# Kernel tuning notes

Hardware: AMD Instinct MI355X
Metric: run time of the kernel (lower is better)

The kernel has to match this reference:

```python
import jax, jax.numpy as jnp
import numpy as np

N_NODES = 100000


def gcn_conv(x, edge_index, W, b):
    """PyG GCNConv: out = D^-1/2 (A+I) D^-1/2 (X W) + b, edge weights = 1."""
    n = x.shape[0]
    h = x @ W  # [N, F_out]
    row, col = edge_index[0], edge_index[1]  # source -> target
    ones = jnp.ones(row.shape[0], dtype=x.dtype)
    # degree on A + I (self loop contributes 1)
    deg = jax.ops.segment_sum(ones, col, num_segments=n) + 1.0
    dinv = jax.lax.rsqrt(deg)  # deg >= 1 so no inf
    norm = dinv[row] * dinv[col]  # [E]
    agg = jax.ops.segment_sum(h[row] * norm[:, None], col, num_segments=n)
    agg = agg + h * (dinv * dinv)[:, None]  # self-loop term
    return agg + b


def setup_inputs() -> dict:
    key = jax.random.key(0)
    ks = jax.random.split(key, 8)
    E = 3200000
    F_in, H, C = 128, 16, 2
    x = jax.random.normal(ks[0], (N_NODES, F_in), dtype=jnp.float32)
    edge_index = jax.random.randint(ks[1], (2, E), 0, N_NODES, dtype=jnp.int64)
    W1 = jax.random.normal(ks[2], (F_in, H), dtype=jnp.float32) * (1.0 / np.sqrt(F_in))
    b1 = jnp.zeros((H,), jnp.float32)
    W2 = jax.random.normal(ks[3], (H, H), dtype=jnp.float32) * (1.0 / np.sqrt(H))
    b2 = jnp.zeros((H,), jnp.float32)
    fc1_W = jax.random.normal(ks[4], (2 * H, H), dtype=jnp.float32) * (1.0 / np.sqrt(2 * H))
    fc1_b = jnp.zeros((H,), jnp.float32)
    fc2_W = jax.random.normal(ks[5], (H, C), dtype=jnp.float32) * (1.0 / np.sqrt(H))
    fc2_b = jnp.zeros((C,), jnp.float32)
    return {"x": x, "edge_index": edge_index, "W1": W1, "b1": b1, "W2": W2,
            "b2": b2, "fc1_W": fc1_W, "fc1_b": fc1_b, "fc2_W": fc2_W, "fc2_b": fc2_b}


def reference(x, edge_index, W1, b1, W2, b2, fc1_W, fc1_b, fc2_W, fc2_b):
    h = jax.nn.relu(gcn_conv(x, edge_index, W1, b1))
    h = jax.nn.relu(gcn_conv(h, edge_index, W2, b2))
    row, col = edge_index[0], edge_index[1]
    ef = jnp.concatenate([h[row], h[col]], axis=1)  # [E, 32]
    ef = jax.nn.relu(ef @ fc1_W + fc1_b)
    logits = ef @ fc2_W + fc2_b  # [E, 2]
    return jax.nn.log_softmax(logits, axis=1)
```

## Files before the change

### kernel.cpp

```cpp
#include <hip/hip_runtime.h>
#include <hip/hip_fp16.h>
#include <cstdint>
#include <cstddef>

#define F_IN 128
#define HID 16
#define NBUK 1024
#define NPB  128
#define CHUNK 8192

__global__ void k_detect(const int* __restrict__ eidx, int* __restrict__ flag) {
    if (blockIdx.x == 0 && threadIdx.x == 0) {
        int all0 = 1;
        for (int i = 0; i < 64; ++i) {
            if (eidx[2 * i + 1] != 0) { all0 = 0; break; }
        }
        *flag = all0;
    }
}

__device__ __forceinline__ int ld_idx(const int* __restrict__ p, int e, int is64) {
    return is64 ? p[2 * e] : p[e];
}

__launch_bounds__(256)
__global__ void k_bhist(const int* __restrict__ eidx, int E,
                        const int* __restrict__ flag, int* __restrict__ ghist) {
    __shared__ int lh[NBUK];
    int t = threadIdx.x;
    for (int i = t; i < NBUK; i += 256) lh[i] = 0;
    __syncthreads();
    int base = blockIdx.x * CHUNK;
    int cnt = min(CHUNK, E - base);
    int is64 = *flag;
    const int* colp = eidx + ((size_t)E << is64);
    for (int i = t; i < cnt; i += 256)
        atomicAdd(&lh[ld_idx(colp, base + i, is64) >> 7], 1);
    __syncthreads();
    for (int i = t; i < NBUK; i += 256)
        if (lh[i]) atomicAdd(&ghist[i], lh[i]);
}

__global__ void k_bscan(const int* __restrict__ ghist, int E,
                        int* __restrict__ boff, int* __restrict__ gcur) {
    __shared__ int s[NBUK];
    int t = threadIdx.x;
    int v = ghist[t];
    s[t] = v;
    __syncthreads();
    for (int off = 1; off < NBUK; off <<= 1) {
        int a = (t >= off) ? s[t - off] : 0;
        __syncthreads();
        s[t] += a;
        __syncthreads();
    }
    int excl = s[t] - v;
    boff[t] = excl;
    gcur[t] = excl;
    if (t == NBUK - 1) boff[NBUK] = E;
}

__launch_bounds__(256)
__global__ void k_bscatter(const int* __restrict__ eidx, int E,
                           const int* __restrict__ flag,
                           int* __restrict__ gcur, uint32_t* __restrict__ pairs) {
    __shared__ int lh[NBUK];
    __shared__ int lcur[NBUK];
    int t = threadIdx.x;
    for (int i = t; i < NBUK; i += 256) lh[i] = 0;
    __syncthreads();
    int base = blockIdx.x * CHUNK;
    int cnt = min(CHUNK, E - base);
    int is64 = *flag;
    const int* rowp = eidx;
    const int* colp = eidx + ((size_t)E << is64);
    for (int i = t; i < cnt; i += 256)
        atomicAdd(&lh[ld_idx(colp, base + i, is64) >> 7], 1);
    __syncthreads();
    for (int i = t; i < NBUK; i += 256) {
        int c = lh[i];
        lcur[i] = c ? atomicAdd(&gcur[i], c) : 0;
    }
    __syncthreads();
    for (int i = t; i < cnt; i += 256) {
        int c = ld_idx(colp, base + i, is64);
        int r = ld_idx(rowp, base + i, is64);
        int buk = c >> 7;
        int pos = atomicAdd(&lcur[buk], 1);
        pairs[pos] = (uint32_t)r | ((uint32_t)(c & 127) << 20);
    }
}

__launch_bounds__(256)
__global__ void k_bsort(const uint32_t* __restrict__ pairs, const int* __restrict__ boff,
                        int* __restrict__ srcs, int* __restrict__ noff,
                        float* __restrict__ dinv, int n) {
    __shared__ int cnt[NPB];
    __shared__ int scn[NPB];
    int t = threadIdx.x;
    int b = blockIdx.x;
    if (t < NPB) cnt[t] = 0;
    __syncthreads();
    int beg = boff[b], end = boff[b + 1];
    for (int k = beg + t; k < end; k += 256)
        atomicAdd(&cnt[pairs[k] >> 20], 1);
    __syncthreads();
    if (t < NPB) scn[t] = cnt[t];
    __syncthreads();
    for (int off = 1; off < NPB; off <<= 1) {
        int v = 0;
        if (t < NPB && t >= off) v = scn[t - off];
        __syncthreads();
        if (t < NPB) scn[t] += v;
        __syncthreads();
    }
    if (t < NPB) {
        int node = b * NPB + t;
        int excl = scn[t] - cnt[t];
        if (node <= n) noff[node] = beg + excl;
        if (node < n)  dinv[node] = rsqrtf((float)cnt[t] + 1.0f);
        cnt[t] = beg + excl;
    }
    __syncthreads();
    for (int k = beg + t; k < end; k += 256) {
        uint32_t p = pairs[k];
        int pos = atomicAdd(&cnt[p >> 20], 1);
        srcs[pos] = (int)(p & 0xFFFFF);
    }
}

__launch_bounds__(256)
__global__ void k_gemm1(const float* __restrict__ x, const float* __restrict__ W1,
                        const float* __restrict__ dinv, __half* __restrict__ hs, int n) {
    __shared__ float Wt[16 * 132];
    for (int i = threadIdx.x; i < F_IN * HID; i += 256) {
        int k = i >> 4, j = i & 15;
        Wt[j * 132 + k] = W1[i];
    }
    __syncthreads();
    int row = blockIdx.x * 16 + (threadIdx.x >> 4);
    int j = threadIdx.x & 15;
    if (row >= n) return;
    const float4* xr = (const float4*)(x + (size_t)row * F_IN);
    float acc = 0.f;
#pragma unroll
    for (int kk = 0; kk < 32; ++kk) {
        float4 xv = xr[kk];
        float4 wv = *(const float4*)&Wt[j * 132 + 4 * kk];
        acc += xv.x * wv.x + xv.y * wv.y + xv.z * wv.z + xv.w * wv.w;
    }
    hs[(size_t)row * HID + j] = __float2half(acc * dinv[row]);
}

template <int EPI>
__launch_bounds__(256)
__global__ void k_layer(const int* __restrict__ srcs, const int* __restrict__ noff,
                        const __half* __restrict__ hs, const float* __restrict__ dinv,
                        const float* __restrict__ bias, const float* __restrict__ Wnext,
                        __half* __restrict__ out0, __half* __restrict__ out1) {
    __shared__ float Ws[512];
    __shared__ float bs[16];
    __shared__ float srow[16 * 17];
    int t = threadIdx.x;
    int nw = (EPI == 0) ? 256 : 512;
    for (int i = t; i < nw; i += 256) Ws[i] = Wnext[i];
    if (t < 16) bs[t] = bias[t];
    __syncthreads();

    int i = blockIdx.x * 16 + (t >> 4);
    int j = t & 15;
    int beg = noff[i], end = noff[i + 1];
    float acc = __half2float(hs[(size_t)i * HID + j]);

    int kb = beg;
    for (; kb + 16 <= end; kb += 16) {
        int idx = srcs[kb + j];
#pragma unroll
        for (int m = 0; m < 16; ++m) {
            int r = __shfl(idx, m, 16);
            acc += __half2float(hs[(size_t)r * HID + j]);
        }
    }
    if (kb < end) {
        int lim = end - kb;
        int idx = srcs[kb + ((j < lim) ? j : (lim - 1))];
        for (int m = 0; m < lim; ++m) {
            int r = __shfl(idx, m, 16);
            acc += __half2float(hs[(size_t)r * HID + j]);
        }
    }

    float di = dinv[i];
    float hrelu = fmaxf(acc * di + bs[j], 0.f);
    int ln = t >> 4;
    __syncthreads();
    srow[ln * 17 + j] = hrelu;
    __syncthreads();
    float a0 = 0.f, a1 = 0.f;
#pragma unroll
    for (int k = 0; k < 16; ++k) {
        float hv = srow[ln * 17 + k];
        a0 += hv * Ws[k * 16 + j];
        if (EPI == 1) a1 += hv * Ws[(16 + k) * 16 + j];
    }
    if (EPI == 0) {
        out0[(size_t)i * HID + j] = __float2half(a0 * di);
    } else {
        out0[(size_t)i * HID + j] = __float2half(a0);
        out1[(size_t)i * HID + j] = __float2half(a1);
    }
}

__launch_bounds__(256)
__global__ void k_edge(const int* __restrict__ eidx, int E, const int* __restrict__ flag,
                       const __half* __restrict__ u, const __half* __restrict__ v,
                       const float* __restrict__ fc1b, const float* __restrict__ fc2W,
                       const float* __restrict__ fc2b, float* __restrict__ out) {
    __shared__ float b1s[16], W2s[32], b2s[2];
    if (threadIdx.x < 16) b1s[threadIdx.x] = fc1b[threadIdx.x];
    if (threadIdx.x < 32) W2s[threadIdx.x] = fc2W[threadIdx.x];
    if (threadIdx.x < 2) b2s[threadIdx.x] = fc2b[threadIdx.x];
    __syncthreads();
    int e = blockIdx.x * blockDim.x + threadIdx.x;
    if (e >= E) return;
    int is64 = *flag;
    const int* rowp = eidx;
    const int* colp = eidx + ((size_t)E << is64);
    int r = ld_idx(rowp, e, is64);
    int c = ld_idx(colp, e, is64);
    const uint4* up = (const uint4*)(u + (size_t)r * HID);
    const uint4* vp = (const uint4*)(v + (size_t)c * HID);
    uint4 U0 = up[0], U1 = up[1], V0 = vp[0], V1 = vp[1];
    float l0 = b2s[0], l1 = b2s[1];
#define PROC(uw, vw, jb)                                                        \
    {                                                                           \
        float2 fu = __half22float2(*(__half2*)&(uw));                           \
        float2 fv = __half22float2(*(__half2*)&(vw));                           \
        float z = fmaxf(fu.x + fv.x + b1s[jb], 0.f);                            \
        l0 += z * W2s[2 * (jb)]; l1 += z * W2s[2 * (jb) + 1];                   \
        z = fmaxf(fu.y + fv.y + b1s[(jb) + 1], 0.f);                            \
        l0 += z * W2s[2 * (jb) + 2]; l1 += z * W2s[2 * (jb) + 3];               \
    }
    PROC(U0.x, V0.x, 0) PROC(U0.y, V0.y, 2) PROC(U0.z, V0.z, 4) PROC(U0.w, V0.w, 6)
    PROC(U1.x, V1.x, 8) PROC(U1.y, V1.y, 10) PROC(U1.z, V1.z, 12) PROC(U1.w, V1.w, 14)
#undef PROC
    float m = fmaxf(l0, l1);
    float e0 = __expf(l0 - m), e1 = __expf(l1 - m);
    float lse = m + __logf(e0 + e1);
    ((float2*)out)[e] = make_float2(l0 - lse, l1 - lse);
}

static inline size_t rnd4(size_t v) { return (v + 3) & ~(size_t)3; }

extern "C" void kernel_launch(void* const* d_in, const int* in_sizes, int n_in,
                              void* d_out, int out_size, void* d_ws, size_t ws_size,
                              hipStream_t stream) {
    const float* x    = (const float*)d_in[0];
    const int*   eidx = (const int*)d_in[1];
    const float* W1   = (const float*)d_in[2];
    const float* b1   = (const float*)d_in[3];
    const float* W2   = (const float*)d_in[4];
    const float* b2   = (const float*)d_in[5];
    const float* fc1W = (const float*)d_in[6];
    const float* fc1b = (const float*)d_in[7];
    const float* fc2W = (const float*)d_in[8];
    const float* fc2b = (const float*)d_in[9];

    const int n = in_sizes[0] / F_IN;
    const int E = in_sizes[1] / 2;
    const int NBLK_SORT = (E + CHUNK - 1) / CHUNK;
    const int NBLK_BUK  = (n + NPB - 1) / NPB;

    float* ws = (float*)d_ws;
    size_t a = 0;
    float*    dinv  = ws + a;              a += rnd4(n);
    uint32_t* pairs = (uint32_t*)(ws + a); a += rnd4(E);
    int*      srcs  = (int*)(ws + a);      a += rnd4(E);
    int*      noff  = (int*)(ws + a);      a += rnd4(n + 1);
    int*      boff  = (int*)(ws + a);      a += rnd4(NBUK + 1);
    int*      gcur  = (int*)(ws + a);      a += NBUK;
    int*      ghist = (int*)(ws + a);      a += NBUK;
    int*      flag  = (int*)(ws + a);      a += 4;
    __half*   hs1   = (__half*)(ws + a);   a += rnd4((size_t)n * HID / 2);
    __half*   hs2   = (__half*)(ws + a);   a += rnd4((size_t)n * HID / 2);
    __half*   ubuf  = (__half*)(ws + a);   a += rnd4((size_t)n * HID / 2);
    __half*   vbuf  = (__half*)(ws + a);   a += rnd4((size_t)n * HID / 2);
    float* out = (float*)d_out;

    k_detect<<<1, 64, 0, stream>>>(eidx, flag);

    hipMemsetAsync(ghist, 0, NBUK * sizeof(int), stream);
    k_bhist<<<NBLK_SORT, 256, 0, stream>>>(eidx, E, flag, ghist);
    k_bscan<<<1, NBUK, 0, stream>>>(ghist, E, boff, gcur);
    k_bscatter<<<NBLK_SORT, 256, 0, stream>>>(eidx, E, flag, gcur, pairs);
    k_bsort<<<NBLK_BUK, 256, 0, stream>>>(pairs, boff, srcs, noff, dinv, n);

    k_gemm1<<<(n + 15) / 16, 256, 0, stream>>>(x, W1, dinv, hs1, n);

    k_layer<0><<<n / 16, 256, 0, stream>>>(srcs, noff, hs1, dinv, b1, W2, hs2, nullptr);
    k_layer<1><<<n / 16, 256, 0, stream>>>(srcs, noff, hs2, dinv, b2, fc1W, ubuf, vbuf);
    k_edge<<<(E + 255) / 256, 256, 0, stream>>>(eidx, E, flag, ubuf, vbuf,
                                                fc1b, fc2W, fc2b, out);
}
```

Baseline: 271.5 us.

## Pack int32 edge list during scatter, use nontemporal accesses, coarsen sort buckets

During the bucket scatter pass, each edge's (row, col) is also written as a packed int32 pair into spare workspace. The edge MLP kernel then reads that packed array instead of the strided int64 edge_index, which cuts the bytes it pulls in. Most streaming loads and stores become nontemporal. Buckets are coarsened from 1024×128 nodes to 256×512 nodes, and the per-bucket sort now runs with 512 threads, so fewer global atomics are needed. A redundant barrier in the layer kernel is also dropped. The costs are an extra write of the edge list and fewer, larger blocks in the bucket sort, which may underfill the GPU.

```diff
diff --git a/kernel.cpp b/kernel.cpp
--- a/kernel.cpp
+++ b/kernel.cpp
@@ -5,9 +5,13 @@
 
 #define F_IN 128
 #define HID 16
-#define NBUK 1024
-#define NPB  128
+#define NBUK 256
+#define NPB  512
 #define CHUNK 8192
+
+typedef float f4v __attribute__((ext_vector_type(4)));
+typedef float f2v __attribute__((ext_vector_type(2)));
+typedef int   i2v __attribute__((ext_vector_type(2)));
 
 __global__ void k_detect(const int* __restrict__ eidx, int* __restrict__ flag) {
     if (blockIdx.x == 0 && threadIdx.x == 0) {
@@ -19,8 +23,9 @@
     }
 }
 
-__device__ __forceinline__ int ld_idx(const int* __restrict__ p, int e, int is64) {
-    return is64 ? p[2 * e] : p[e];
+__device__ __forceinline__ int ld_idx_nt(const int* __restrict__ p, int e, int is64) {
+    return is64 ? __builtin_nontemporal_load(&p[2 * e])
+                : __builtin_nontemporal_load(&p[e]);
 }
 
 __launch_bounds__(256)
@@ -28,17 +33,16 @@
                         const int* __restrict__ flag, int* __restrict__ ghist) {
     __shared__ int lh[NBUK];
     int t = threadIdx.x;
-    for (int i = t; i < NBUK; i += 256) lh[i] = 0;
+    if (t < NBUK) lh[t] = 0;
     __syncthreads();
     int base = blockIdx.x * CHUNK;
     int cnt = min(CHUNK, E - base);
     int is64 = *flag;
     const int* colp = eidx + ((size_t)E << is64);
     for (int i = t; i < cnt; i += 256)
-        atomicAdd(&lh[ld_idx(colp, base + i, is64) >> 7], 1);
-    __syncthreads();
-    for (int i = t; i < NBUK; i += 256)
-        if (lh[i]) atomicAdd(&ghist[i], lh[i]);
+        atomicAdd(&lh[ld_idx_nt(colp, base + i, is64) >> 9], 1);
+    __syncthreads();
+    if (t < NBUK && lh[t]) atomicAdd(&ghist[t], lh[t]);
 }
 
 __global__ void k_bscan(const int* __restrict__ ghist, int E,
@@ -63,11 +67,12 @@
 __launch_bounds__(256)
 __global__ void k_bscatter(const int* __restrict__ eidx, int E,
                            const int* __restrict__ flag,
-                           int* __restrict__ gcur, uint32_t* __restrict__ pairs) {
+                           int* __restrict__ gcur, uint32_t* __restrict__ pairs,
+                           i2v* __restrict__ epack) {
     __shared__ int lh[NBUK];
     __shared__ int lcur[NBUK];
     int t = threadIdx.x;
-    for (int i = t; i < NBUK; i += 256) lh[i] = 0;
+    if (t < NBUK) lh[t] = 0;
     __syncthreads();
     int base = blockIdx.x * CHUNK;
     int cnt = min(CHUNK, E - base);
@@ -75,23 +80,28 @@
     const int* rowp = eidx;
     const int* colp = eidx + ((size_t)E << is64);
     for (int i = t; i < cnt; i += 256)
-        atomicAdd(&lh[ld_idx(colp, base + i, is64) >> 7], 1);
-    __syncthreads();
-    for (int i = t; i < NBUK; i += 256) {
-        int c = lh[i];
-        lcur[i] = c ? atomicAdd(&gcur[i], c) : 0;
+        atomicAdd(&lh[ld_idx_nt(colp, base + i, is64) >> 9], 1);
+    __syncthreads();
+    if (t < NBUK) {
+        int c = lh[t];
+        lcur[t] = c ? atomicAdd(&gcur[t], c) : 0;
     }
     __syncthreads();
     for (int i = t; i < cnt; i += 256) {
-        int c = ld_idx(colp, base + i, is64);
-        int r = ld_idx(rowp, base + i, is64);
-        int buk = c >> 7;
+        int e = base + i;
+        int c = ld_idx_nt(colp, e, is64);
+        int r = ld_idx_nt(rowp, e, is64);
+        if (epack) {
+            i2v pk; pk.x = r; pk.y = c;
+            __builtin_nontemporal_store(pk, &epack[e]);
+        }
+        int buk = c >> 9;
         int pos = atomicAdd(&lcur[buk], 1);
-        pairs[pos] = (uint32_t)r | ((uint32_t)(c & 127) << 20);
-    }
-}
-
-__launch_bounds__(256)
+        pairs[pos] = (uint32_t)r | ((uint32_t)(c & (NPB - 1)) << 20);
+    }
+}
+
+__launch_bounds__(512)
 __global__ void k_bsort(const uint32_t* __restrict__ pairs, const int* __restrict__ boff,
                         int* __restrict__ srcs, int* __restrict__ noff,
                         float* __restrict__ dinv, int n) {
@@ -99,30 +109,27 @@
     __shared__ int scn[NPB];
     int t = threadIdx.x;
     int b = blockIdx.x;
-    if (t < NPB) cnt[t] = 0;
+    cnt[t] = 0;
     __syncthreads();
     int beg = boff[b], end = boff[b + 1];
-    for (int k = beg + t; k < end; k += 256)
+    for (int k = beg + t; k < end; k += 512)
         atomicAdd(&cnt[pairs[k] >> 20], 1);
     __syncthreads();
-    if (t < NPB) scn[t] = cnt[t];
+    scn[t] = cnt[t];
     __syncthreads();
     for (int off = 1; off < NPB; off <<= 1) {
-        int v = 0;
-        if (t < NPB && t >= off) v = scn[t - off];
+        int v = (t >= off) ? scn[t - off] : 0;
         __syncthreads();
-        if (t < NPB) scn[t] += v;
+        scn[t] += v;
         __syncthreads();
     }
-    if (t < NPB) {
-        int node = b * NPB + t;
-        int excl = scn[t] - cnt[t];
-        if (node <= n) noff[node] = beg + excl;
-        if (node < n)  dinv[node] = rsqrtf((float)cnt[t] + 1.0f);
-        cnt[t] = beg + excl;
-    }
-    __syncthreads();
-    for (int k = beg + t; k < end; k += 256) {
+    int node = b * NPB + t;
+    int excl = scn[t] - cnt[t];
+    if (node <= n) noff[node] = beg + excl;
+    if (node < n)  dinv[node] = rsqrtf((float)cnt[t] + 1.0f);
+    cnt[t] = beg + excl;
+    __syncthreads();
+    for (int k = beg + t; k < end; k += 512) {
         uint32_t p = pairs[k];
         int pos = atomicAdd(&cnt[p >> 20], 1);
         srcs[pos] = (int)(p & 0xFFFFF);
@@ -141,11 +148,11 @@
     int row = blockIdx.x * 16 + (threadIdx.x >> 4);
     int j = threadIdx.x & 15;
     if (row >= n) return;
-    const float4* xr = (const float4*)(x + (size_t)row * F_IN);
+    const f4v* xr = (const f4v*)(x + (size_t)row * F_IN);
     float acc = 0.f;
 #pragma unroll
     for (int kk = 0; kk < 32; ++kk) {
-        float4 xv = xr[kk];
+        f4v xv = __builtin_nontemporal_load(&xr[kk]);
         float4 wv = *(const float4*)&Wt[j * 132 + 4 * kk];
         acc += xv.x * wv.x + xv.y * wv.y + xv.z * wv.z + xv.w * wv.w;
     }
@@ -174,7 +181,7 @@
 
     int kb = beg;
     for (; kb + 16 <= end; kb += 16) {
-        int idx = srcs[kb + j];
+        int idx = __builtin_nontemporal_load(&srcs[kb + j]);
 #pragma unroll
         for (int m = 0; m < 16; ++m) {
             int r = __shfl(idx, m, 16);
@@ -193,7 +200,6 @@
     float di = dinv[i];
     float hrelu = fmaxf(acc * di + bs[j], 0.f);
     int ln = t >> 4;
-    __syncthreads();
     srow[ln * 17 + j] = hrelu;
     __syncthreads();
     float a0 = 0.f, a1 = 0.f;
@@ -211,8 +217,10 @@
     }
 }
 
-__launch_bounds__(256)
-__global__ void k_edge(const int* __restrict__ eidx, int E, const int* __restrict__ flag,
+template <int USE_EPACK>
+__launch_bounds__(256)
+__global__ void k_edge(const int* __restrict__ eidx, const i2v* __restrict__ epack,
+                       int E, const int* __restrict__ flag,
                        const __half* __restrict__ u, const __half* __restrict__ v,
                        const float* __restrict__ fc1b, const float* __restrict__ fc2W,
                        const float* __restrict__ fc2b, float* __restrict__ out) {
@@ -223,11 +231,17 @@
     __syncthreads();
     int e = blockIdx.x * blockDim.x + threadIdx.x;
     if (e >= E) return;
-    int is64 = *flag;
-    const int* rowp = eidx;
-    const int* colp = eidx + ((size_t)E << is64);
-    int r = ld_idx(rowp, e, is64);
-    int c = ld_idx(colp, e, is64);
+    int r, c;
+    if (USE_EPACK) {
+        i2v pk = __builtin_nontemporal_load(&epack[e]);
+        r = pk.x; c = pk.y;
+    } else {
+        int is64 = *flag;
+        const int* rowp = eidx;
+        const int* colp = eidx + ((size_t)E << is64);
+        r = ld_idx_nt(rowp, e, is64);
+        c = ld_idx_nt(colp, e, is64);
+    }
     const uint4* up = (const uint4*)(u + (size_t)r * HID);
     const uint4* vp = (const uint4*)(v + (size_t)c * HID);
     uint4 U0 = up[0], U1 = up[1], V0 = vp[0], V1 = vp[1];
@@ -247,7 +261,8 @@
     float m = fmaxf(l0, l1);
     float e0 = __expf(l0 - m), e1 = __expf(l1 - m);
     float lse = m + __logf(e0 + e1);
-    ((float2*)out)[e] = make_float2(l0 - lse, l1 - lse);
+    f2v res; res.x = l0 - lse; res.y = l1 - lse;
+    __builtin_nontemporal_store(res, &((f2v*)out)[e]);
 }
 
 static inline size_t rnd4(size_t v) { return (v + 3) & ~(size_t)3; }
@@ -285,20 +300,26 @@
     __half*   hs2   = (__half*)(ws + a);   a += rnd4((size_t)n * HID / 2);
     __half*   ubuf  = (__half*)(ws + a);   a += rnd4((size_t)n * HID / 2);
     __half*   vbuf  = (__half*)(ws + a);   a += rnd4((size_t)n * HID / 2);
+    bool use_epack = ws_size >= (a + 2 * (size_t)E + 8) * sizeof(float);
+    i2v* epack = use_epack ? (i2v*)(ws + a) : nullptr;
     float* out = (float*)d_out;
 
     k_detect<<<1, 64, 0, stream>>>(eidx, flag);
 
-    hipMemsetAsync(ghist, 0, NBUK * sizeof(int), stream);
+    (void)hipMemsetAsync(ghist, 0, NBUK * sizeof(int), stream);
     k_bhist<<<NBLK_SORT, 256, 0, stream>>>(eidx, E, flag, ghist);
     k_bscan<<<1, NBUK, 0, stream>>>(ghist, E, boff, gcur);
-    k_bscatter<<<NBLK_SORT, 256, 0, stream>>>(eidx, E, flag, gcur, pairs);
-    k_bsort<<<NBLK_BUK, 256, 0, stream>>>(pairs, boff, srcs, noff, dinv, n);
+    k_bscatter<<<NBLK_SORT, 256, 0, stream>>>(eidx, E, flag, gcur, pairs, epack);
+    k_bsort<<<NBLK_BUK, 512, 0, stream>>>(pairs, boff, srcs, noff, dinv, n);
 
     k_gemm1<<<(n + 15) / 16, 256, 0, stream>>>(x, W1, dinv, hs1, n);
 
     k_layer<0><<<n / 16, 256, 0, stream>>>(srcs, noff, hs1, dinv, b1, W2, hs2, nullptr);
     k_layer<1><<<n / 16, 256, 0, stream>>>(srcs, noff, hs2, dinv, b2, fc1W, ubuf, vbuf);
-    k_edge<<<(E + 255) / 256, 256, 0, stream>>>(eidx, E, flag, ubuf, vbuf,
-                                                fc1b, fc2W, fc2b, out);
-}
+    if (use_epack)
+        k_edge<1><<<(E + 255) / 256, 256, 0, stream>>>(eidx, epack, E, flag, ubuf, vbuf,
+                                                       fc1b, fc2W, fc2b, out);
+    else
+        k_edge<0><<<(E + 255) / 256, 256, 0, stream>>>(eidx, epack, E, flag, ubuf, vbuf,
+                                                       fc1b, fc2W, fc2b, out);
+}
```

Measured after the change: 325.7 us. 20.0% more time.
